# Kernel tuning notes

Hardware: AMD Instinct MI355X
Metric: run time of the kernel (lower is better)

## Reference

```python
import math
import jax, jax.numpy as jnp
import numpy as np

B, N, C = 2, 2048, 768
H, DH = 12, 64  # num_heads, head_dim


def setup_inputs() -> dict:
    key = jax.random.key(0)
    ks = jax.random.split(key, 5)
    s = 1.0 / math.sqrt(C)  # keep linear outputs O(1)
    return {
        "x": jax.random.normal(ks[0], (B, N, C), jnp.float32),
        "Wq": jax.random.normal(ks[1], (C, C), jnp.float32) * s,
        "bq": jnp.zeros((C,), jnp.float32),
        "Wk": jax.random.normal(ks[2], (C, C), jnp.float32) * s,
        "bk": jnp.zeros((C,), jnp.float32),
        "Wv": jax.random.normal(ks[3], (C, C), jnp.float32) * s,
        "bv": jnp.zeros((C,), jnp.float32),
        "Wp": jax.random.normal(ks[4], (C, C), jnp.float32) * s,
        "bp": jnp.zeros((C,), jnp.float32),
    }


def reference(x, Wq, bq, Wk, bk, Wv, bv, Wp, bp):
    # Linear projections; torch nn.Linear computes x @ W.T + b, here W stored
    # as (in, out) so it's x @ W + b with equivalent math.
    def split(t):  # [B,N,C] -> [B,H,N,DH]
        return t.reshape(B, N, H, DH).transpose(0, 2, 1, 3)

    q = split(x @ Wq + bq)
    k = split(x @ Wk + bk)
    v = split(x @ Wv + bv)
    scale = 1.0 / math.sqrt(DH)
    attn = jnp.einsum("bhqd,bhkd->bhqk", q, k) * scale  # [B,H,N,N]
    attn = jax.nn.softmax(attn, axis=-1)  # attn_drop=0.0 -> identity
    y = jnp.einsum("bhqk,bhkd->bhqd", attn, v)  # [B,H,N,DH]
    y = y.transpose(0, 2, 1, 3).reshape(B, N, C)
    return y @ Wp + bp  # proj_drop=0.0 -> identity
```

## Files before the change

### kernel.cpp

```cpp
#include <hip/hip_runtime.h>


typedef __bf16 bf16_t;
typedef __bf16 bf16x8 __attribute__((ext_vector_type(8)));
typedef __bf16 bf16x4 __attribute__((ext_vector_type(4)));
typedef short  short4_t __attribute__((ext_vector_type(4)));
typedef float  floatx4 __attribute__((ext_vector_type(4)));

#define MFMA32(a, b, c) __builtin_amdgcn_mfma_f32_16x16x32_bf16(a, b, c, 0, 0, 0)
#define MFMA16(a, b, c) __builtin_amdgcn_mfma_f32_16x16x16bf16_1k(a, b, c, 0, 0, 0)

__device__ __forceinline__ void gload16(const bf16_t* g, bf16_t* l) {
  __builtin_amdgcn_global_load_lds(
      (__attribute__((address_space(1))) void*)g,
      (__attribute__((address_space(3))) void*)l, 16, 0, 0);
}

__global__ __launch_bounds__(256) void cvt_all_kernel(
    const float* __restrict__ x, const float* __restrict__ W0,
    const float* __restrict__ W1, const float* __restrict__ W2,
    const float* __restrict__ W3, bf16_t* __restrict__ xb,
    bf16_t* __restrict__ T0, bf16_t* __restrict__ T1,
    bf16_t* __restrict__ T2, bf16_t* __restrict__ T3) {
  __shared__ bf16_t T[64][65];
  const int id = blockIdx.x;
  if (id < 3072) {
    int i = id * 256 + threadIdx.x;
    floatx4 v = ((const floatx4*)x)[i];
    bf16x4 o;
    o[0] = (bf16_t)v[0]; o[1] = (bf16_t)v[1]; o[2] = (bf16_t)v[2]; o[3] = (bf16_t)v[3];
    ((bf16x4*)xb)[i] = o;
    return;
  }
  const int wid = id - 3072;
  const int z = wid / 144, rem = wid % 144;
  const int by = rem / 12, bx = rem % 12;
  const float* W = (z == 0) ? W0 : (z == 1) ? W1 : (z == 2) ? W2 : W3;
  bf16_t* WT = (z == 0) ? T0 : (z == 1) ? T1 : (z == 2) ? T2 : T3;
  const int c = threadIdx.x & 63, r0 = threadIdx.x >> 6;
  const int i0 = by * 64, o0 = bx * 64;
#pragma unroll
  for (int p = 0; p < 16; ++p) {
    int r = p * 4 + r0;
    T[r][c] = (bf16_t)W[(i0 + r) * 768 + o0 + c];
  }
  __syncthreads();
#pragma unroll
  for (int p = 0; p < 16; ++p) {
    int r = p * 4 + r0;
    WT[(o0 + r) * 768 + i0 + c] = T[c][r];
  }
}

#define LDPG 72


#define LOADSET(A0, A1, A2, A3, B0, B1, B2, B3, KT)        \
  A0 = *(const bf16x8*)(gA + (KT));                        \
  A1 = *(const bf16x8*)(gA + (KT) + 32 * 768);             \
  A2 = *(const bf16x8*)(gA + (KT) + 64 * 768);             \
  A3 = *(const bf16x8*)(gA + (KT) + 96 * 768);             \
  B0 = *(const bf16x8*)(gB + (KT));                        \
  B1 = *(const bf16x8*)(gB + (KT) + 32 * 768);             \
  B2 = *(const bf16x8*)(gB + (KT) + 64 * 768);             \
  B3 = *(const bf16x8*)(gB + (KT) + 96 * 768);

#define WRITESET(A0, A1, A2, A3, B0, B1, B2, B3)           \
  *(bf16x8*)(lA) = A0;                                     \
  *(bf16x8*)(lA + 32 * LDPG) = A1;                         \
  *(bf16x8*)(lA + 64 * LDPG) = A2;                         \
  *(bf16x8*)(lA + 96 * LDPG) = A3;                         \
  *(bf16x8*)(lB) = B0;                                     \
  *(bf16x8*)(lB + 32 * LDPG) = B1;                         \
  *(bf16x8*)(lB + 64 * LDPG) = B2;                         \
  *(bf16x8*)(lB + 96 * LDPG) = B3;

#define GCOMPUTE()                                                          \
  {                                                                         \
    bf16x8 af[4], bfr[4];                                                   \
    _Pragma("unroll") for (int i = 0; i < 4; ++i) {                         \
      af[i]  = *(bf16x8*)&Al[(wr * 64 + i * 16 + l15) * LDPG + kk2 * 32 + quad * 8]; \
      bfr[i] = *(bf16x8*)&Bl[(wc * 64 + i * 16 + l15) * LDPG + kk2 * 32 + quad * 8]; \
    }                                                                       \
    _Pragma("unroll") for (int mi = 0; mi < 4; ++mi)                        \
        _Pragma("unroll") for (int ni = 0; ni < 4; ++ni)                    \
            acc[mi][ni] = MFMA32(af[mi], bfr[ni], acc[mi][ni]);             \
  }

#define GCOMPUTE2()                                \
  _Pragma("unroll") for (int kk2 = 0; kk2 < 2; ++kk2) GCOMPUTE()

__global__ __launch_bounds__(256, 2) void gemm_qkv(
    const bf16_t* __restrict__ Xb, const bf16_t* __restrict__ WqT,
    const bf16_t* __restrict__ WkT, const bf16_t* __restrict__ WvT,
    const float* __restrict__ bq, const float* __restrict__ bk,
    const float* __restrict__ bv, bf16_t* __restrict__ qw,
    bf16_t* __restrict__ kw, bf16_t* __restrict__ vtw) {
  __shared__ bf16_t Al[128 * LDPG];
  __shared__ bf16_t Bl[128 * LDPG];
  const int z = blockIdx.z;
  const bf16_t* Wt = (z == 0) ? WqT : (z == 1) ? WkT : WvT;
  const float* bias = (z == 0) ? bq : (z == 1) ? bk : bv;
  const float oscale = (z == 0) ? 0.18033688011112042f : 1.0f;

  const int tid = threadIdx.x, lane = tid & 63, w = tid >> 6;
  const int wr = w >> 1, wc = w & 1;
  const int l15 = lane & 15, quad = lane >> 4;
  const int m0 = blockIdx.y * 128, n0 = blockIdx.x * 128;

  const int r0 = tid >> 3, q0c = (tid & 7) * 8;
  const bf16_t* gA = &Wt[(m0 + r0) * 768 + q0c];
  const bf16_t* gB = &Xb[(n0 + r0) * 768 + q0c];
  bf16_t* lA = &Al[r0 * LDPG + q0c];
  bf16_t* lB = &Bl[r0 * LDPG + q0c];

  floatx4 acc[4][4] = {};
  bf16x8 pa0, pa1, pa2, pa3, pb0, pb1, pb2, pb3;
  bf16x8 qa0, qa1, qa2, qa3, qb0, qb1, qb2, qb3;

  LOADSET(pa0, pa1, pa2, pa3, pb0, pb1, pb2, pb3, 0);
  for (int kt = 0; kt < 768; kt += 128) {
    WRITESET(pa0, pa1, pa2, pa3, pb0, pb1, pb2, pb3);
    __syncthreads();
    LOADSET(qa0, qa1, qa2, qa3, qb0, qb1, qb2, qb3, kt + 64);
    GCOMPUTE2();
    __syncthreads();
    WRITESET(qa0, qa1, qa2, qa3, qb0, qb1, qb2, qb3);
    __syncthreads();
    if (kt + 128 < 768) LOADSET(pa0, pa1, pa2, pa3, pb0, pb1, pb2, pb3, kt + 128);
    GCOMPUTE2();
    __syncthreads();
  }

  const int hh = (m0 + wr * 64) >> 6;
#pragma unroll
  for (int mi = 0; mi < 4; ++mi) {
    const int d0 = mi * 16 + quad * 4;
    const int gm0 = m0 + wr * 64 + d0;
    float bv4[4];
#pragma unroll
    for (int r = 0; r < 4; ++r) bv4[r] = bias[gm0 + r];
#pragma unroll
    for (int ni = 0; ni < 4; ++ni) {
      const int gn = n0 + wc * 64 + ni * 16 + l15;
      const int bb = gn >> 11, tok = gn & 2047;
      const int bh = bb * 12 + hh;
      if (z == 0) {
        bf16x4 pk;
#pragma unroll
        for (int r = 0; r < 4; ++r)
          pk[r] = (bf16_t)((acc[mi][ni][r] + bv4[r]) * oscale);
        *(bf16x4*)&qw[bh * 131072 + tok * 64 + d0] = pk;
      } else if (z == 1) {
        const int kt2 = tok >> 7, k128 = tok & 127;
        const int nk = k128 >> 4, kl15 = k128 & 15;
        const int kk = d0 >> 5, kq = (d0 >> 3) & 3, j0 = d0 & 7;
        bf16x4 pk;
#pragma unroll
        for (int r = 0; r < 4; ++r)
          pk[r] = (bf16_t)(acc[mi][ni][r] + bv4[r]);
        *(bf16x4*)&kw[bh * 131072 + kt2 * 8192 +
                      ((nk * 2 + kk) * 64 + kq * 16 + kl15) * 8 + j0] = pk;
      } else {
        const int kt2 = tok >> 7, k128 = tok & 127;
        const int nk = k128 >> 4, vq = (k128 >> 2) & 3, j = k128 & 3;
        const int nd = d0 >> 4, vl0 = d0 & 15;
        const int base = bh * 131072 + kt2 * 8192 +
                         ((nk * 4 + nd) * 64 + vq * 16 + vl0) * 4 + j;
#pragma unroll
        for (int r = 0; r < 4; ++r)
          vtw[base + r * 4] = (bf16_t)(acc[mi][ni][r] + bv4[r]);
      }
    }
  }
}

__global__ __launch_bounds__(256, 2) void gemm_proj(
    const bf16_t* __restrict__ Yb, const bf16_t* __restrict__ WpT,
    const float* __restrict__ bias, float* __restrict__ out) {
  __shared__ bf16_t Al[128 * LDPG];
  __shared__ bf16_t Bl[128 * LDPG];
  const int tid = threadIdx.x, lane = tid & 63, w = tid >> 6;
  const int wr = w >> 1, wc = w & 1;
  const int l15 = lane & 15, quad = lane >> 4;
  const int m0 = blockIdx.y * 128, n0 = blockIdx.x * 128;

  const int r0 = tid >> 3, q0c = (tid & 7) * 8;
  const bf16_t* gA = &WpT[(m0 + r0) * 768 + q0c];
  const bf16_t* gB = &Yb[(n0 + r0) * 768 + q0c];
  bf16_t* lA = &Al[r0 * LDPG + q0c];
  bf16_t* lB = &Bl[r0 * LDPG + q0c];

  floatx4 acc[4][4] = {};
  bf16x8 pa0, pa1, pa2, pa3, pb0, pb1, pb2, pb3;
  bf16x8 qa0, qa1, qa2, qa3, qb0, qb1, qb2, qb3;

  LOADSET(pa0, pa1, pa2, pa3, pb0, pb1, pb2, pb3, 0);
  for (int kt = 0; kt < 768; kt += 128) {
    WRITESET(pa0, pa1, pa2, pa3, pb0, pb1, pb2, pb3);
    __syncthreads();
    LOADSET(qa0, qa1, qa2, qa3, qb0, qb1, qb2, qb3, kt + 64);
    GCOMPUTE2();
    __syncthreads();
    WRITESET(qa0, qa1, qa2, qa3, qb0, qb1, qb2, qb3);
    __syncthreads();
    if (kt + 128 < 768) LOADSET(pa0, pa1, pa2, pa3, pb0, pb1, pb2, pb3, kt + 128);
    GCOMPUTE2();
    __syncthreads();
  }

#pragma unroll
  for (int mi = 0; mi < 4; ++mi) {
    const int gm0 = m0 + wr * 64 + mi * 16 + quad * 4;
    floatx4 bv4;
#pragma unroll
    for (int r = 0; r < 4; ++r) bv4[r] = bias[gm0 + r];
#pragma unroll
    for (int ni = 0; ni < 4; ++ni) {
      const int gn = n0 + wc * 64 + ni * 16 + l15;
      floatx4 v = acc[mi][ni] + bv4;
      *(floatx4*)&out[gn * 768 + gm0] = v;
    }
  }
}

__global__ __launch_bounds__(256, 4) void attn_kernel(
    const bf16_t* __restrict__ Q, const bf16_t* __restrict__ Kf,
    const bf16_t* __restrict__ Vf, bf16_t* __restrict__ Y) {
  __shared__ __align__(16) bf16_t smem[16384];
  __shared__ float Ls[2][2][2][16];
  float* Ox = (float*)smem;

  const int tid = threadIdx.x, lane = tid & 63, w = tid >> 6;
  const int wq = w & 1, wk = w >> 1;
  const int l15 = lane & 15, quad = lane >> 4;

  const int i = blockIdx.x;
  const int xcd = i & 7, j = i >> 3;
  const int bh = xcd * 3 + (j >> 5);
  const int q0 = (j & 31) * 64;

  const bf16_t* Qb = Q + bh * 131072;
  const bf16_t* Kg = Kf + bh * 131072 + tid * 8;
  const bf16_t* Vg = Vf + bh * 131072 + tid * 8;

  bf16x8 qf[2][2];
#pragma unroll
  for (int ni = 0; ni < 2; ++ni)
#pragma unroll
    for (int kk = 0; kk < 2; ++kk)
      qf[ni][kk] = *(const bf16x8*)&Qb[(q0 + wq * 32 + ni * 16 + l15) * 64 +
                                       kk * 32 + quad * 8];

  floatx4 oacc[2][4] = {};
  floatx4 sacc[2] = {};
  const short4_t ones = {0x3F80, 0x3F80, 0x3F80, 0x3F80};

  auto stage = [&](int b, int t) {
    const bf16_t* kg = Kg + t * 4096;
    const bf16_t* vg = Vg + t * 4096;
    bf16_t* kl = smem + b * 8192 + tid * 8;
    bf16_t* vl = smem + b * 8192 + 4096 + tid * 8;
    gload16(kg, kl);
    gload16(kg + 2048, kl + 2048);
    gload16(vg, vl);
    gload16(vg + 2048, vl + 2048);
  };

  auto compute = [&](int b) {
    const bf16_t* Kl = smem + b * 8192;
    const bf16_t* Vl = smem + b * 8192 + 4096;
    short4_t pk[2][2];
#pragma unroll
    for (int mt = 0; mt < 2; ++mt) {
      floatx4 s[2] = {};
#pragma unroll
      for (int kk = 0; kk < 2; ++kk) {
        bf16x8 kfr = *(const bf16x8*)&Kl[((wk * 2 + mt) * 2 + kk) * 512 + lane * 8];
#pragma unroll
        for (int ni = 0; ni < 2; ++ni)
          s[ni] = MFMA32(kfr, qf[ni][kk], s[ni]);
      }
#pragma unroll
      for (int ni = 0; ni < 2; ++ni) {
        bf16x4 ph;
#pragma unroll
        for (int r = 0; r < 4; ++r)
          ph[r] = (bf16_t)__builtin_amdgcn_exp2f(s[ni][r]);
        pk[mt][ni] = __builtin_bit_cast(short4_t, ph);
      }
    }
#pragma unroll
    for (int mt = 0; mt < 2; ++mt) {
#pragma unroll
      for (int nd = 0; nd < 4; ++nd) {
        bf16x4 vfr = *(const bf16x4*)&Vl[((wk * 2 + mt) * 4 + nd) * 256 + lane * 4];
        short4_t vs = __builtin_bit_cast(short4_t, vfr);
#pragma unroll
        for (int ni = 0; ni < 2; ++ni)
          oacc[ni][nd] = MFMA16(pk[mt][ni], vs, oacc[ni][nd]);
      }
#pragma unroll
      for (int ni = 0; ni < 2; ++ni)
        sacc[ni] = MFMA16(pk[mt][ni], ones, sacc[ni]);
    }
  };

  stage(0, 0);
  __syncthreads();
  for (int t = 0; t < 32; t += 2) {
    stage(1, t + 1);
    compute(0);
    __syncthreads();
    if (t + 2 < 32) stage(0, t + 2);
    compute(1);
    __syncthreads();
  }

  if (l15 == 0) {
#pragma unroll
    for (int ni = 0; ni < 2; ++ni)
#pragma unroll
      for (int r = 0; r < 4; ++r)
        Ls[wq][wk][ni][quad * 4 + r] = sacc[ni][r];
  }

#pragma unroll
  for (int ni = 0; ni < 2; ++ni)
#pragma unroll
    for (int ndl = 0; ndl < 2; ++ndl) {
      const int nd = (1 - wk) * 2 + ndl;
      *(floatx4*)&Ox[((((wq * 2 + wk) * 2 + ni) * 2 + ndl) * 64 + lane) * 4] =
          oacc[ni][nd];
    }
  __syncthreads();

  const int bb = bh / 12, h = bh % 12;
#pragma unroll
  for (int ni = 0; ni < 2; ++ni) {
    float tot[4];
#pragma unroll
    for (int r = 0; r < 4; ++r)
      tot[r] = Ls[wq][0][ni][quad * 4 + r] + Ls[wq][1][ni][quad * 4 + r];
#pragma unroll
    for (int ndl = 0; ndl < 2; ++ndl) {
      const int nd = wk * 2 + ndl;
      floatx4 o = oacc[ni][nd];
      floatx4 other =
          *(floatx4*)&Ox[((((wq * 2 + (1 - wk)) * 2 + ni) * 2 + ndl) * 64 + lane) * 4];
      o += other;
#pragma unroll
      for (int r = 0; r < 4; ++r) {
        const int tok = q0 + wq * 32 + ni * 16 + quad * 4 + r;
        const int col = h * 64 + nd * 16 + l15;
        Y[(bb * 2048 + tok) * 768 + col] = (bf16_t)(o[r] / tot[r]);
      }
    }
  }
}

extern "C" void kernel_launch(void* const* d_in, const int* in_sizes, int n_in,
                              void* d_out, int out_size, void* d_ws, size_t ws_size,
                              hipStream_t stream) {
  const float* x  = (const float*)d_in[0];
  const float* Wq = (const float*)d_in[1];
  const float* bq = (const float*)d_in[2];
  const float* Wk = (const float*)d_in[3];
  const float* bk = (const float*)d_in[4];
  const float* Wv = (const float*)d_in[5];
  const float* bv = (const float*)d_in[6];
  const float* Wp = (const float*)d_in[7];
  const float* bp = (const float*)d_in[8];
  float* out = (float*)d_out;

  char* ws = (char*)d_ws;
  bf16_t* xb  = (bf16_t*)ws; ws += (size_t)4096 * 768 * 2;
  bf16_t* WqT = (bf16_t*)ws; ws += (size_t)768 * 768 * 2;
  bf16_t* WkT = (bf16_t*)ws; ws += (size_t)768 * 768 * 2;
  bf16_t* WvT = (bf16_t*)ws; ws += (size_t)768 * 768 * 2;
  bf16_t* WpT = (bf16_t*)ws; ws += (size_t)768 * 768 * 2;
  bf16_t* qw  = (bf16_t*)ws; ws += (size_t)24 * 2048 * 64 * 2;
  bf16_t* kw  = (bf16_t*)ws; ws += (size_t)24 * 2048 * 64 * 2;
  bf16_t* vtw = (bf16_t*)ws; ws += (size_t)24 * 2048 * 64 * 2;
  bf16_t* yw  = (bf16_t*)ws; ws += (size_t)4096 * 768 * 2;

  cvt_all_kernel<<<3648, 256, 0, stream>>>(x, Wq, Wk, Wv, Wp, xb, WqT, WkT, WvT, WpT);
  gemm_qkv<<<dim3(32, 6, 3), 256, 0, stream>>>(xb, WqT, WkT, WvT, bq, bk, bv, qw, kw, vtw);
  attn_kernel<<<768, 256, 0, stream>>>(qw, kw, vtw, yw);
  gemm_proj<<<dim3(32, 6), 256, 0, stream>>>(yw, WpT, bp, out);
}
```

Measured before the change: 173.8 us.

## Fuse x fp32-to-bf16 conversion into QKV GEMM loads; add MFMA priority hints

```diff
diff --git a/kernel.cpp b/kernel.cpp
--- a/kernel.cpp
+++ b/kernel.cpp
@@ -16,29 +16,24 @@
       (__attribute__((address_space(3))) void*)l, 16, 0, 0);
 }
 
-__global__ __launch_bounds__(256) void cvt_all_kernel(
-    const float* __restrict__ x, const float* __restrict__ W0,
-    const float* __restrict__ W1, const float* __restrict__ W2,
-    const float* __restrict__ W3, bf16_t* __restrict__ xb,
+__device__ __forceinline__ bf16x8 cvt8(floatx4 a, floatx4 b) {
+  bf16x8 r;
+  r[0] = (bf16_t)a[0]; r[1] = (bf16_t)a[1]; r[2] = (bf16_t)a[2]; r[3] = (bf16_t)a[3];
+  r[4] = (bf16_t)b[0]; r[5] = (bf16_t)b[1]; r[6] = (bf16_t)b[2]; r[7] = (bf16_t)b[3];
+  return r;
+}
+
+__global__ __launch_bounds__(256) void cvt_wt_kernel(
+    const float* __restrict__ W0, const float* __restrict__ W1,
+    const float* __restrict__ W2, const float* __restrict__ W3,
     bf16_t* __restrict__ T0, bf16_t* __restrict__ T1,
     bf16_t* __restrict__ T2, bf16_t* __restrict__ T3) {
-  __shared__ bf16_t T[64][65];
-  const int id = blockIdx.x;
-  if (id < 3072) {
-    int i = id * 256 + threadIdx.x;
-    floatx4 v = ((const floatx4*)x)[i];
-    bf16x4 o;
-    o[0] = (bf16_t)v[0]; o[1] = (bf16_t)v[1]; o[2] = (bf16_t)v[2]; o[3] = (bf16_t)v[3];
-    ((bf16x4*)xb)[i] = o;
-    return;
-  }
-  const int wid = id - 3072;
-  const int z = wid / 144, rem = wid % 144;
-  const int by = rem / 12, bx = rem % 12;
+  const int z = blockIdx.z;
   const float* W = (z == 0) ? W0 : (z == 1) ? W1 : (z == 2) ? W2 : W3;
   bf16_t* WT = (z == 0) ? T0 : (z == 1) ? T1 : (z == 2) ? T2 : T3;
+  __shared__ bf16_t T[64][65];
   const int c = threadIdx.x & 63, r0 = threadIdx.x >> 6;
-  const int i0 = by * 64, o0 = bx * 64;
+  const int i0 = blockIdx.y * 64, o0 = blockIdx.x * 64;
 #pragma unroll
   for (int p = 0; p < 16; ++p) {
     int r = p * 4 + r0;
@@ -54,26 +49,6 @@
 
 #define LDPG 72
 
-
-#define LOADSET(A0, A1, A2, A3, B0, B1, B2, B3, KT)        \
-  A0 = *(const bf16x8*)(gA + (KT));                        \
-  A1 = *(const bf16x8*)(gA + (KT) + 32 * 768);             \
-  A2 = *(const bf16x8*)(gA + (KT) + 64 * 768);             \
-  A3 = *(const bf16x8*)(gA + (KT) + 96 * 768);             \
-  B0 = *(const bf16x8*)(gB + (KT));                        \
-  B1 = *(const bf16x8*)(gB + (KT) + 32 * 768);             \
-  B2 = *(const bf16x8*)(gB + (KT) + 64 * 768);             \
-  B3 = *(const bf16x8*)(gB + (KT) + 96 * 768);
-
-#define WRITESET(A0, A1, A2, A3, B0, B1, B2, B3)           \
-  *(bf16x8*)(lA) = A0;                                     \
-  *(bf16x8*)(lA + 32 * LDPG) = A1;                         \
-  *(bf16x8*)(lA + 64 * LDPG) = A2;                         \
-  *(bf16x8*)(lA + 96 * LDPG) = A3;                         \
-  *(bf16x8*)(lB) = B0;                                     \
-  *(bf16x8*)(lB + 32 * LDPG) = B1;                         \
-  *(bf16x8*)(lB + 64 * LDPG) = B2;                         \
-  *(bf16x8*)(lB + 96 * LDPG) = B3;
 
 #define GCOMPUTE()                                                          \
   {                                                                         \
@@ -90,8 +65,32 @@
 #define GCOMPUTE2()                                \
   _Pragma("unroll") for (int kk2 = 0; kk2 < 2; ++kk2) GCOMPUTE()
 
+#define LOADSET_Q(A0, A1, A2, A3, F0a, F0b, F1a, F1b, F2a, F2b, F3a, F3b, KT) \
+  A0 = *(const bf16x8*)(gA + (KT));                        \
+  A1 = *(const bf16x8*)(gA + (KT) + 32 * 768);             \
+  A2 = *(const bf16x8*)(gA + (KT) + 64 * 768);             \
+  A3 = *(const bf16x8*)(gA + (KT) + 96 * 768);             \
+  F0a = *(const floatx4*)(gBf + (KT));                     \
+  F0b = *(const floatx4*)(gBf + (KT) + 4);                 \
+  F1a = *(const floatx4*)(gBf + (KT) + 32 * 768);          \
+  F1b = *(const floatx4*)(gBf + (KT) + 32 * 768 + 4);      \
+  F2a = *(const floatx4*)(gBf + (KT) + 64 * 768);          \
+  F2b = *(const floatx4*)(gBf + (KT) + 64 * 768 + 4);      \
+  F3a = *(const floatx4*)(gBf + (KT) + 96 * 768);          \
+  F3b = *(const floatx4*)(gBf + (KT) + 96 * 768 + 4);
+
+#define WRITESET_Q(A0, A1, A2, A3, F0a, F0b, F1a, F1b, F2a, F2b, F3a, F3b) \
+  *(bf16x8*)(lA) = A0;                                     \
+  *(bf16x8*)(lA + 32 * LDPG) = A1;                         \
+  *(bf16x8*)(lA + 64 * LDPG) = A2;                         \
+  *(bf16x8*)(lA + 96 * LDPG) = A3;                         \
+  *(bf16x8*)(lB) = cvt8(F0a, F0b);                         \
+  *(bf16x8*)(lB + 32 * LDPG) = cvt8(F1a, F1b);             \
+  *(bf16x8*)(lB + 64 * LDPG) = cvt8(F2a, F2b);             \
+  *(bf16x8*)(lB + 96 * LDPG) = cvt8(F3a, F3b);
+
 __global__ __launch_bounds__(256, 2) void gemm_qkv(
-    const bf16_t* __restrict__ Xb, const bf16_t* __restrict__ WqT,
+    const float* __restrict__ Xf, const bf16_t* __restrict__ WqT,
     const bf16_t* __restrict__ WkT, const bf16_t* __restrict__ WvT,
     const float* __restrict__ bq, const float* __restrict__ bk,
     const float* __restrict__ bv, bf16_t* __restrict__ qw,
@@ -110,24 +109,30 @@
 
   const int r0 = tid >> 3, q0c = (tid & 7) * 8;
   const bf16_t* gA = &Wt[(m0 + r0) * 768 + q0c];
-  const bf16_t* gB = &Xb[(n0 + r0) * 768 + q0c];
+  const float* gBf = &Xf[(n0 + r0) * 768 + q0c];
   bf16_t* lA = &Al[r0 * LDPG + q0c];
   bf16_t* lB = &Bl[r0 * LDPG + q0c];
 
   floatx4 acc[4][4] = {};
-  bf16x8 pa0, pa1, pa2, pa3, pb0, pb1, pb2, pb3;
-  bf16x8 qa0, qa1, qa2, qa3, qb0, qb1, qb2, qb3;
-
-  LOADSET(pa0, pa1, pa2, pa3, pb0, pb1, pb2, pb3, 0);
+  bf16x8 pa0, pa1, pa2, pa3;
+  floatx4 pf0a, pf0b, pf1a, pf1b, pf2a, pf2b, pf3a, pf3b;
+  bf16x8 qa0, qa1, qa2, qa3;
+  floatx4 qf0a, qf0b, qf1a, qf1b, qf2a, qf2b, qf3a, qf3b;
+
+  LOADSET_Q(pa0, pa1, pa2, pa3, pf0a, pf0b, pf1a, pf1b, pf2a, pf2b, pf3a, pf3b, 0);
   for (int kt = 0; kt < 768; kt += 128) {
-    WRITESET(pa0, pa1, pa2, pa3, pb0, pb1, pb2, pb3);
-    __syncthreads();
-    LOADSET(qa0, qa1, qa2, qa3, qb0, qb1, qb2, qb3, kt + 64);
+    WRITESET_Q(pa0, pa1, pa2, pa3, pf0a, pf0b, pf1a, pf1b, pf2a, pf2b, pf3a, pf3b);
+    __syncthreads();
+    LOADSET_Q(qa0, qa1, qa2, qa3, qf0a, qf0b, qf1a, qf1b, qf2a, qf2b, qf3a, qf3b,
+              kt + 64);
     GCOMPUTE2();
     __syncthreads();
-    WRITESET(qa0, qa1, qa2, qa3, qb0, qb1, qb2, qb3);
-    __syncthreads();
-    if (kt + 128 < 768) LOADSET(pa0, pa1, pa2, pa3, pb0, pb1, pb2, pb3, kt + 128);
+    WRITESET_Q(qa0, qa1, qa2, qa3, qf0a, qf0b, qf1a, qf1b, qf2a, qf2b, qf3a, qf3b);
+    __syncthreads();
+    if (kt + 128 < 768) {
+      LOADSET_Q(pa0, pa1, pa2, pa3, pf0a, pf0b, pf1a, pf1b, pf2a, pf2b, pf3a, pf3b,
+                kt + 128);
+    }
     GCOMPUTE2();
     __syncthreads();
   }
@@ -175,6 +180,26 @@
   }
 }
 
+#define LOADSET(A0, A1, A2, A3, B0, B1, B2, B3, KT)        \
+  A0 = *(const bf16x8*)(gA + (KT));                        \
+  A1 = *(const bf16x8*)(gA + (KT) + 32 * 768);             \
+  A2 = *(const bf16x8*)(gA + (KT) + 64 * 768);             \
+  A3 = *(const bf16x8*)(gA + (KT) + 96 * 768);             \
+  B0 = *(const bf16x8*)(gB + (KT));                        \
+  B1 = *(const bf16x8*)(gB + (KT) + 32 * 768);             \
+  B2 = *(const bf16x8*)(gB + (KT) + 64 * 768);             \
+  B3 = *(const bf16x8*)(gB + (KT) + 96 * 768);
+
+#define WRITESET(A0, A1, A2, A3, B0, B1, B2, B3)           \
+  *(bf16x8*)(lA) = A0;                                     \
+  *(bf16x8*)(lA + 32 * LDPG) = A1;                         \
+  *(bf16x8*)(lA + 64 * LDPG) = A2;                         \
+  *(bf16x8*)(lA + 96 * LDPG) = A3;                         \
+  *(bf16x8*)(lB) = B0;                                     \
+  *(bf16x8*)(lB + 32 * LDPG) = B1;                         \
+  *(bf16x8*)(lB + 64 * LDPG) = B2;                         \
+  *(bf16x8*)(lB + 96 * LDPG) = B3;
+
 __global__ __launch_bounds__(256, 2) void gemm_proj(
     const bf16_t* __restrict__ Yb, const bf16_t* __restrict__ WpT,
     const float* __restrict__ bias, float* __restrict__ out) {
@@ -274,6 +299,7 @@
 #pragma unroll
     for (int mt = 0; mt < 2; ++mt) {
       floatx4 s[2] = {};
+      __builtin_amdgcn_s_setprio(1);
 #pragma unroll
       for (int kk = 0; kk < 2; ++kk) {
         bf16x8 kfr = *(const bf16x8*)&Kl[((wk * 2 + mt) * 2 + kk) * 512 + lane * 8];
@@ -281,6 +307,7 @@
         for (int ni = 0; ni < 2; ++ni)
           s[ni] = MFMA32(kfr, qf[ni][kk], s[ni]);
       }
+      __builtin_amdgcn_s_setprio(0);
 #pragma unroll
       for (int ni = 0; ni < 2; ++ni) {
         bf16x4 ph;
@@ -290,6 +317,7 @@
         pk[mt][ni] = __builtin_bit_cast(short4_t, ph);
       }
     }
+    __builtin_amdgcn_s_setprio(1);
 #pragma unroll
     for (int mt = 0; mt < 2; ++mt) {
 #pragma unroll
@@ -304,6 +332,7 @@
       for (int ni = 0; ni < 2; ++ni)
         sacc[ni] = MFMA16(pk[mt][ni], ones, sacc[ni]);
     }
+    __builtin_amdgcn_s_setprio(0);
   };
 
   stage(0, 0);
@@ -374,7 +403,6 @@
   float* out = (float*)d_out;
 
   char* ws = (char*)d_ws;
-  bf16_t* xb  = (bf16_t*)ws; ws += (size_t)4096 * 768 * 2;
   bf16_t* WqT = (bf16_t*)ws; ws += (size_t)768 * 768 * 2;
   bf16_t* WkT = (bf16_t*)ws; ws += (size_t)768 * 768 * 2;
   bf16_t* WvT = (bf16_t*)ws; ws += (size_t)768 * 768 * 2;
@@ -384,8 +412,8 @@
   bf16_t* vtw = (bf16_t*)ws; ws += (size_t)24 * 2048 * 64 * 2;
   bf16_t* yw  = (bf16_t*)ws; ws += (size_t)4096 * 768 * 2;
 
-  cvt_all_kernel<<<3648, 256, 0, stream>>>(x, Wq, Wk, Wv, Wp, xb, WqT, WkT, WvT, WpT);
-  gemm_qkv<<<dim3(32, 6, 3), 256, 0, stream>>>(xb, WqT, WkT, WvT, bq, bk, bv, qw, kw, vtw);
+  cvt_wt_kernel<<<dim3(12, 12, 4), 256, 0, stream>>>(Wq, Wk, Wv, Wp, WqT, WkT, WvT, WpT);
+  gemm_qkv<<<dim3(32, 6, 3), 256, 0, stream>>>(x, WqT, WkT, WvT, bq, bk, bv, qw, kw, vtw);
   attn_kernel<<<768, 256, 0, stream>>>(qw, kw, vtw, yw);
   gemm_proj<<<dim3(32, 6), 256, 0, stream>>>(yw, WpT, bp, out);
 }
```

Result: slower. 182.6 us (+5.0%).
